# Performance work log

Hardware: AMD Instinct MI355X
Metric: run time of the kernel (lower is better)

The kernel has to match this reference:

```python
import jax, jax.numpy as jnp
import numpy as np

N_NODES = 100000


def _gcn_layer(x, W, b, src, dst, inv_sqrt_deg):
    # transform first (cheaper when out_dim <= in_dim), then normalized aggregate
    h = x @ W  # [N, out]
    coeff = (inv_sqrt_deg[src] * inv_sqrt_deg[dst])[:, None]  # [E,1] sym norm
    msgs = h[src] * coeff  # [E, out]
    agg = jax.ops.segment_sum(msgs, dst, num_segments=N_NODES)  # [N, out]
    return agg + b


def setup_inputs() -> dict:
    key = jax.random.key(0)
    ks = jax.random.split(key, 8)
    n, e = N_NODES, 1600000
    x = jax.random.normal(ks[0], (n, 256), dtype=jnp.float32)
    src = jax.random.randint(ks[1], (e,), 0, n)
    dst = jax.random.randint(ks[2], (e,), 0, n)
    W1 = jax.random.normal(ks[3], (256, 128), dtype=jnp.float32) * 0.05
    b1 = jax.random.normal(ks[4], (128,), dtype=jnp.float32) * 0.05
    W2 = jax.random.normal(ks[5], (128, 40), dtype=jnp.float32) * 0.05
    b2 = jax.random.normal(ks[6], (40,), dtype=jnp.float32) * 0.05
    return {"x": x, "src": src, "dst": dst, "W1": W1, "b1": b1, "W2": W2, "b2": b2}


def reference(x, src, dst, W1, b1, W2, b2):
    # degree-based symmetric normalization D^{-1/2} A D^{-1/2}
    ones = jnp.ones(src.shape, dtype=x.dtype)
    deg = jax.ops.segment_sum(ones, dst, num_segments=N_NODES)
    inv_sqrt_deg = jnp.where(deg > 0, jax.lax.rsqrt(jnp.maximum(deg, 1.0)), 0.0)
    h = _gcn_layer(x, W1, b1, src, dst, inv_sqrt_deg)
    h = jax.nn.relu(h)
    h = _gcn_layer(h, W2, b2, src, dst, inv_sqrt_deg)
    return h
```

## Files before the change

### kernel.cpp

```cpp
#include <hip/hip_runtime.h>
#include <hip/hip_bf16.h>


#define CHUNK   4096
#define NPB     512
#define NBUCK   196
#define BBCAP   9216

typedef __bf16 bf16x8 __attribute__((ext_vector_type(8)));
typedef float floatx4 __attribute__((ext_vector_type(4)));

__device__ inline unsigned short f2bf(float f) {
    unsigned u = __float_as_uint(f);
    u += 0x7FFF + ((u >> 16) & 1);
    return (unsigned short)(u >> 16);
}
__device__ inline float bflo(unsigned p) { return __uint_as_float(p << 16); }
__device__ inline float bfhi(unsigned p) { return __uint_as_float(p & 0xFFFF0000u); }

__global__ __launch_bounds__(256) void k_part(const int* __restrict__ src,
                                              const int* __restrict__ dst,
                                              int* __restrict__ gcursor,
                                              unsigned* __restrict__ buckets, int E) {
    __shared__ unsigned srec[CHUNK];
    __shared__ unsigned char sb8[CHUNK];
    __shared__ int hist[NBUCK];
    __shared__ int lbase[NBUCK];
    __shared__ int gbase[NBUCK];
    __shared__ int scanbuf[256];
    int t = threadIdx.x;
    int base = blockIdx.x * CHUNK;
    int cnt = min(CHUNK, E - base);
    for (int i = t; i < NBUCK; i += 256) hist[i] = 0;
    __syncthreads();

    unsigned rec[16];
    unsigned br[16];
    bool valid[4];
    #pragma unroll
    for (int k = 0; k < 4; ++k) {
        int e0 = k * 1024 + t * 4;
        valid[k] = (e0 < cnt);
        if (valid[k]) {
            int4 s4 = *(const int4*)&src[base + e0];
            int4 d4 = *(const int4*)&dst[base + e0];
            int ss[4] = {s4.x, s4.y, s4.z, s4.w};
            int dd[4] = {d4.x, d4.y, d4.z, d4.w};
            #pragma unroll
            for (int j = 0; j < 4; ++j) {
                int b = dd[j] >> 9;
                int r = atomicAdd(&hist[b], 1);
                rec[k * 4 + j] = (unsigned)ss[j] | ((unsigned)(dd[j] & 511) << 17);
                br[k * 4 + j] = (unsigned)b | ((unsigned)r << 8);
            }
        }
    }
    __syncthreads();
    scanbuf[t] = (t < NBUCK) ? hist[t] : 0;
    __syncthreads();
    for (int s = 1; s < 256; s <<= 1) {
        int v = (t >= s) ? scanbuf[t - s] : 0;
        __syncthreads();
        scanbuf[t] += v;
        __syncthreads();
    }
    if (t < NBUCK) {
        lbase[t] = scanbuf[t] - hist[t];
        gbase[t] = atomicAdd(&gcursor[t], hist[t]);
    }
    __syncthreads();
    #pragma unroll
    for (int k = 0; k < 4; ++k) {
        if (valid[k]) {
            #pragma unroll
            for (int j = 0; j < 4; ++j) {
                unsigned b = br[k * 4 + j] & 255u;
                unsigned r = br[k * 4 + j] >> 8;
                int p = lbase[b] + (int)r;
                srec[p] = rec[k * 4 + j];
                sb8[p] = (unsigned char)b;
            }
        }
    }
    __syncthreads();
    for (int i = t; i < cnt; i += 256) {
        int b = sb8[i];
        int pos = gbase[b] + (i - lbase[b]);
        if (pos < BBCAP) buckets[(size_t)b * BBCAP + pos] = srec[i];
    }
}

__global__ __launch_bounds__(256) void k_count(const unsigned* __restrict__ buckets,
                                               const int* __restrict__ gcursor,
                                               int* __restrict__ deg, int N) {
    __shared__ int hist[NPB];
    int b = blockIdx.x;
    for (int i = threadIdx.x; i < NPB; i += 256) hist[i] = 0;
    __syncthreads();
    int cnt = min(gcursor[b], BBCAP);
    const unsigned* bk = &buckets[(size_t)b * BBCAP];
    for (int i = threadIdx.x; i < cnt; i += 256)
        atomicAdd(&hist[bk[i] >> 17], 1);
    __syncthreads();
    int node0 = b << 9;
    for (int i = threadIdx.x; i < NPB; i += 256)
        if (node0 + i < N) deg[node0 + i] = hist[i];
}

__global__ void k_isd_offsets(const int* __restrict__ deg, float* __restrict__ isd,
                              int* __restrict__ offsets, int* __restrict__ counter, int N) {
    int n = blockIdx.x * blockDim.x + threadIdx.x;
    int lane = threadIdx.x & 63;
    int d = (n < N) ? deg[n] : 0;
    if (n <= N) isd[n] = (d > 0) ? rsqrtf((float)d) : 0.f;
    int dp = (d + 15) & ~15;
    int pref = dp;
    #pragma unroll
    for (int sh = 1; sh < 64; sh <<= 1) {
        int t = __shfl_up(pref, sh);
        if (lane >= sh) pref += t;
    }
    int total = __shfl(pref, 63);
    int base = 0;
    if (lane == 63) base = atomicAdd(counter, total);
    base = __shfl(base, 63);
    if (n < N) offsets[n] = base + pref - dp;
}

__global__ __launch_bounds__(256) void k_place(const unsigned* __restrict__ buckets,
                                               const int* __restrict__ gcursor,
                                               const int* __restrict__ offsets,
                                               const int* __restrict__ deg,
                                               int* __restrict__ csr, int N) {
    __shared__ int cur[NPB];
    int b = blockIdx.x;
    int node0 = b << 9;
    for (int i = threadIdx.x; i < NPB; i += 256)
        cur[i] = (node0 + i < N) ? offsets[node0 + i] : 0;
    __syncthreads();
    int cnt = min(gcursor[b], BBCAP);
    const unsigned* bk = &buckets[(size_t)b * BBCAP];
    for (int i = threadIdx.x; i < cnt; i += 256) {
        unsigned r = bk[i];
        int p = atomicAdd(&cur[r >> 17], 1);
        csr[p] = (int)(r & 0x1FFFFu);
    }
    __syncthreads();
    for (int i = threadIdx.x; i < NPB; i += 256) {
        int n = node0 + i;
        if (n < N) {
            int d = deg[n];
            int st = offsets[n] + d;
            int en = offsets[n] + ((d + 15) & ~15);
            for (int p = st; p < en; ++p) csr[p] = N;
        }
    }
}

__global__ void k_prep_w1(const float* __restrict__ W1, unsigned short* __restrict__ w1s,
                          unsigned* __restrict__ h2z) {
    if (blockIdx.x == 0 && threadIdx.x < 36) h2z[threadIdx.x] = 0;
    int flat = blockIdx.x * 256 + threadIdx.x;
    int kt = flat >> 9;
    int nt = (flat >> 6) & 7;
    int lane = flat & 63;
    int kbase = kt * 32 + ((lane >> 4) << 3);
    int n = nt * 16 + (lane & 15);
    unsigned short v[8];
    #pragma unroll
    for (int j = 0; j < 8; ++j) v[j] = f2bf(W1[(size_t)(kbase + j) * 128 + n]);
    unsigned short* d = &w1s[(size_t)flat * 8];
    *(short4*)(d)     = make_short4(v[0], v[1], v[2], v[3]);
    *(short4*)(d + 4) = make_short4(v[4], v[5], v[6], v[7]);
}

__global__ __launch_bounds__(256) void k_gemm1(const float* __restrict__ X,
                                               const unsigned short* __restrict__ w1s,
                                               const float* __restrict__ isd,
                                               unsigned short* __restrict__ H, int N) {
    __shared__ __align__(16) unsigned short smem[8192];
    unsigned short* sA = smem;
    unsigned short* sB = smem + 2048;
    int tid = threadIdx.x;
    int lane = tid & 63;
    int wave = tid >> 6;
    int wr = wave >> 1;
    int wc = wave & 1;
    int m0 = blockIdx.x * 64;

    floatx4 acc[2][4] = {};

    for (int kt = 0; kt < 8; ++kt) {
        #pragma unroll
        for (int i = 0; i < 2; ++i) {
            int f = tid * 2 + i;
            int row = f >> 3;
            int c4 = (f & 7) * 4;
            float4 v = make_float4(0.f, 0.f, 0.f, 0.f);
            int grow = m0 + row;
            if (grow < N) v = *(const float4*)&X[(size_t)grow * 256 + kt * 32 + c4];
            int mt = row >> 4;
            int flane = (row & 15) | ((c4 >> 3) << 4);
            int j0 = c4 & 7;
            unsigned short* d = &sA[(size_t)(mt * 64 + flane) * 8 + j0];
            *(short4*)d = make_short4(f2bf(v.x), f2bf(v.y), f2bf(v.z), f2bf(v.w));
        }
        {
            const float4* srcp = (const float4*)&w1s[(size_t)kt * 4096];
            float4* dstp = (float4*)sB;
            dstp[tid] = srcp[tid];
            dstp[tid + 256] = srcp[tid + 256];
        }
        __syncthreads();
        bf16x8 a[2], b[4];
        #pragma unroll
        for (int p = 0; p < 2; ++p)
            a[p] = *(const bf16x8*)&sA[(size_t)((wr * 2 + p) * 64 + lane) * 8];
        #pragma unroll
        for (int q = 0; q < 4; ++q)
            b[q] = *(const bf16x8*)&sB[(size_t)((wc * 4 + q) * 64 + lane) * 8];
        #pragma unroll
        for (int p = 0; p < 2; ++p)
            #pragma unroll
            for (int q = 0; q < 4; ++q)
                acc[p][q] = __builtin_amdgcn_mfma_f32_16x16x32_bf16(a[p], b[q], acc[p][q], 0, 0, 0);
        __syncthreads();
    }
    float sc[2][4];
    #pragma unroll
    for (int p = 0; p < 2; ++p)
        #pragma unroll
        for (int r = 0; r < 4; ++r) {
            int g = m0 + wr * 32 + p * 16 + ((lane >> 4) << 2) + r;
            sc[p][r] = isd[g > N ? N : g];
        }
    #pragma unroll
    for (int p = 0; p < 2; ++p)
        #pragma unroll
        for (int q = 0; q < 4; ++q)
            #pragma unroll
            for (int r = 0; r < 4; ++r) {
                int rl = wr * 32 + p * 16 + ((lane >> 4) << 2) + r;
                int c = wc * 64 + q * 16 + (lane & 15);
                smem[rl * 128 + c] = f2bf(acc[p][q][r] * sc[p][r]);
            }
    __syncthreads();
    #pragma unroll
    for (int i = 0; i < 4; ++i) {
        int f = tid + i * 256;
        int row = f >> 4;
        int c8 = (f & 15) * 8;
        int grow = m0 + row;
        if (grow <= N)
            *(float4*)&H[(size_t)grow * 128 + c8] = *(const float4*)&smem[row * 128 + c8];
    }
}

__global__ __launch_bounds__(256) void k_agg1(const unsigned* __restrict__ Hu,
                                              const int* __restrict__ csr,
                                              const float* __restrict__ isd,
                                              const int* __restrict__ offsets,
                                              const int* __restrict__ deg,
                                              const float* __restrict__ b1,
                                              unsigned* __restrict__ H1u, int N) {
    int node = __builtin_amdgcn_readfirstlane((blockIdx.x * blockDim.x + threadIdx.x) >> 6);
    int lane = threadIdx.x & 63;
    if (node >= N) return;
    int start = offsets[node];
    int nb = (deg[node] + 15) >> 4;
    float isdn = isd[node];
    float acc0 = 0.f, acc1 = 0.f;
    for (int ib = 0; ib < nb; ++ib) {
        int b0 = start + ib * 16;
        int s[16];
        #pragma unroll
        for (int j = 0; j < 16; ++j) s[j] = csr[b0 + j];
        unsigned p[16];
        #pragma unroll
        for (int j = 0; j < 16; ++j) p[j] = Hu[(size_t)s[j] * 64 + lane];
        #pragma unroll
        for (int j = 0; j < 16; ++j) {
            acc0 += bflo(p[j]);
            acc1 += bfhi(p[j]);
        }
    }
    float r0 = fmaxf(fmaf(isdn, acc0, b1[2 * lane]), 0.f);
    float r1 = fmaxf(fmaf(isdn, acc1, b1[2 * lane + 1]), 0.f);
    H1u[(size_t)node * 64 + lane] = (unsigned)f2bf(r0) | ((unsigned)f2bf(r1) << 16);
}

__global__ __launch_bounds__(256) void k_gemm2(const unsigned short* __restrict__ H1,
                                               const float* __restrict__ W2,
                                               const float* __restrict__ isd,
                                               unsigned short* __restrict__ H2, int N) {
    __shared__ float sH[64][132];
    __shared__ float sW[128 * 40];
    int tid = threadIdx.x;
    int block_row = blockIdx.x * 64;
    for (int i = tid; i < 64 * 16; i += 256) {
        int r = i >> 4;
        int c8 = (i & 15) * 8;
        int grow = block_row + r;
        uint4 v = make_uint4(0, 0, 0, 0);
        if (grow < N) v = *(const uint4*)&H1[(size_t)grow * 128 + c8];
        float* d = &sH[r][c8];
        d[0] = bflo(v.x); d[1] = bfhi(v.x);
        d[2] = bflo(v.y); d[3] = bfhi(v.y);
        d[4] = bflo(v.z); d[5] = bfhi(v.z);
        d[6] = bflo(v.w); d[7] = bfhi(v.w);
    }
    for (int i = tid; i < 1280; i += 256)
        *(float4*)&sW[i * 4] = *(const float4*)&W2[(size_t)i * 4];
    __syncthreads();

    int row = tid >> 2;
    int c0 = (tid & 3) * 10;
    float acc[10] = {};
    for (int k = 0; k < 128; ++k) {
        float hv = sH[row][k];
        #pragma unroll
        for (int j = 0; j < 5; ++j) {
            float2 wv = *(const float2*)&sW[k * 40 + c0 + 2 * j];
            acc[2 * j]     = fmaf(hv, wv.x, acc[2 * j]);
            acc[2 * j + 1] = fmaf(hv, wv.y, acc[2 * j + 1]);
        }
    }
    int grow = block_row + row;
    if (grow < N) {
        float scn = isd[grow];
        unsigned* o = (unsigned*)&H2[(size_t)grow * 40 + c0];
        #pragma unroll
        for (int j = 0; j < 5; ++j)
            o[j] = (unsigned)f2bf(acc[2 * j] * scn) |
                   ((unsigned)f2bf(acc[2 * j + 1] * scn) << 16);
    }
}

__global__ __launch_bounds__(256) void k_agg2(const unsigned* __restrict__ Hu2,
                                              const int* __restrict__ csr,
                                              const float* __restrict__ isd,
                                              const int* __restrict__ offsets,
                                              const int* __restrict__ deg,
                                              const float* __restrict__ b2,
                                              float* __restrict__ out, int N) {
    int node = __builtin_amdgcn_readfirstlane((blockIdx.x * blockDim.x + threadIdx.x) >> 6);
    int lane = threadIdx.x & 63;
    if (node >= N) return;
    int start = offsets[node];
    int nb = (deg[node] + 15) >> 4;
    float isdn = isd[node];
    int sub = lane >> 5;
    int c = lane & 31;
    float acc0 = 0.f, acc1 = 0.f;
    for (int ib = 0; ib < nb; ++ib) {
        int b0 = start + ib * 16;
        #pragma unroll
        for (int j = 0; j < 8; ++j) {
            int s = csr[b0 + (j << 1) + sub];
            unsigned q = Hu2[(size_t)s * 20 + c];
            acc0 += bflo(q);
            acc1 += bfhi(q);
        }
    }
    acc0 += __shfl(acc0, lane + 32);
    acc1 += __shfl(acc1, lane + 32);
    if (lane < 20)
        *(float2*)&out[(size_t)node * 40 + 2 * lane] =
            make_float2(fmaf(isdn, acc0, b2[2 * lane]), fmaf(isdn, acc1, b2[2 * lane + 1]));
}

extern "C" void kernel_launch(void* const* d_in, const int* in_sizes, int n_in,
                              void* d_out, int out_size, void* d_ws, size_t ws_size,
                              hipStream_t stream) {
    const float* x  = (const float*)d_in[0];
    const int*  src = (const int*)d_in[1];
    const int*  dst = (const int*)d_in[2];
    const float* W1 = (const float*)d_in[3];
    const float* b1 = (const float*)d_in[4];
    const float* W2 = (const float*)d_in[5];
    const float* b2 = (const float*)d_in[6];
    float* out = (float*)d_out;

    const int N = in_sizes[0] / 256;
    const int E = in_sizes[1];

    char* w = (char*)d_ws;
    auto alloc = [&](size_t bytes) -> void* {
        void* p = (void*)w;
        w += (bytes + 15) & ~(size_t)15;
        return p;
    };
    int*      gcursor = (int*)alloc(256 * 4);
    int*      counter = (int*)alloc(16);
    int*      deg     = (int*)alloc((size_t)N * 4);
    float*    isd     = (float*)alloc((size_t)(N + 1) * 4);
    int*      offsets = (int*)alloc((size_t)(N + 1) * 4);
    unsigned* buckets = (unsigned*)alloc((size_t)NBUCK * BBCAP * 4);
    int*      csr     = (int*)alloc((size_t)(E + 16 * (size_t)N) * 4);
    unsigned short* w1s = (unsigned short*)alloc(32768 * 2);
    unsigned short* h   = (unsigned short*)alloc((size_t)(N + 1) * 128 * 2);
    unsigned short* h1  = (unsigned short*)alloc((size_t)N * 128 * 2);
    unsigned short* h2  = (unsigned short*)alloc(((size_t)(N + 1) * 20 + 16) * 4);

    hipMemsetAsync(gcursor, 0, 256 * 4 + 16, stream);

    int nchunk = (E + CHUNK - 1) / CHUNK;
    k_part<<<nchunk, 256, 0, stream>>>(src, dst, gcursor, buckets, E);
    k_count<<<NBUCK, 256, 0, stream>>>(buckets, gcursor, deg, N);
    k_isd_offsets<<<(N + 256) / 256, 256, 0, stream>>>(deg, isd, offsets, counter, N);
    k_place<<<NBUCK, 256, 0, stream>>>(buckets, gcursor, offsets, deg, csr, N);
    k_prep_w1<<<16, 256, 0, stream>>>(W1, w1s, (unsigned*)h2 + (size_t)N * 20);
    k_gemm1<<<(N + 63) / 64, 256, 0, stream>>>(x, w1s, isd, h, N);
    k_agg1<<<(N + 3) / 4, 256, 0, stream>>>((const unsigned*)h, csr, isd, offsets, deg,
                                            b1, (unsigned*)h1, N);
    k_gemm2<<<(N + 63) / 64, 256, 0, stream>>>(h1, W2, isd, h2, N);
    k_agg2<<<(N + 3) / 4, 256, 0, stream>>>((const unsigned*)h2, csr, isd, offsets, deg,
                                            b2, out, N);
}
```

Measured before the change: 408.4 us.

## Fuse graph preprocessing kernels and run CSR placement concurrently with GEMM1

Degree counting moves into the partition kernel as global atomics, and the W1 prep blocks become extra blocks of that kernel. Offset scan, isd and CSR placement merge into one kernel whose remaining blocks run GEMM1, which now computes its row scales from deg itself. This cuts the launch count from six to two and lets the irregular CSR build overlap the dense GEMM. The cost is 1.6M scattered global atomics on deg, a larger memset, and offsets that depend on the order buckets grab the shared counter.

Result: slower. 432.8 us (+6.0%).

```diff
diff --git a/kernel.cpp b/kernel.cpp
--- a/kernel.cpp
+++ b/kernel.cpp
@@ -18,17 +18,39 @@
 __device__ inline float bflo(unsigned p) { return __uint_as_float(p << 16); }
 __device__ inline float bfhi(unsigned p) { return __uint_as_float(p & 0xFFFF0000u); }
 
-__global__ __launch_bounds__(256) void k_part(const int* __restrict__ src,
-                                              const int* __restrict__ dst,
-                                              int* __restrict__ gcursor,
-                                              unsigned* __restrict__ buckets, int E) {
+__global__ __launch_bounds__(256) void k_f1(const int* __restrict__ src,
+                                            const int* __restrict__ dst,
+                                            int* __restrict__ gcursor,
+                                            unsigned* __restrict__ buckets,
+                                            int* __restrict__ deg,
+                                            int E, int nchunk,
+                                            const float* __restrict__ W1,
+                                            unsigned short* __restrict__ w1s,
+                                            unsigned* __restrict__ h2z) {
+    int t = threadIdx.x;
+    if ((int)blockIdx.x >= nchunk) {
+        int pb = blockIdx.x - nchunk;
+        if (pb == 0 && t < 36) h2z[t] = 0;
+        int flat = pb * 256 + t;
+        int kt = flat >> 9;
+        int nt = (flat >> 6) & 7;
+        int lane = flat & 63;
+        int kbase = kt * 32 + ((lane >> 4) << 3);
+        int n = nt * 16 + (lane & 15);
+        unsigned short v[8];
+        #pragma unroll
+        for (int j = 0; j < 8; ++j) v[j] = f2bf(W1[(size_t)(kbase + j) * 128 + n]);
+        unsigned short* d = &w1s[(size_t)flat * 8];
+        *(short4*)(d)     = make_short4(v[0], v[1], v[2], v[3]);
+        *(short4*)(d + 4) = make_short4(v[4], v[5], v[6], v[7]);
+        return;
+    }
     __shared__ unsigned srec[CHUNK];
     __shared__ unsigned char sb8[CHUNK];
     __shared__ int hist[NBUCK];
     __shared__ int lbase[NBUCK];
     __shared__ int gbase[NBUCK];
     __shared__ int scanbuf[256];
-    int t = threadIdx.x;
     int base = blockIdx.x * CHUNK;
     int cnt = min(CHUNK, E - base);
     for (int i = t; i < NBUCK; i += 256) hist[i] = 0;
@@ -50,6 +72,7 @@
             for (int j = 0; j < 4; ++j) {
                 int b = dd[j] >> 9;
                 int r = atomicAdd(&hist[b], 1);
+                atomicAdd(&deg[dd[j]], 1);
                 rec[k * 4 + j] = (unsigned)ss[j] | ((unsigned)(dd[j] & 511) << 17);
                 br[k * 4 + j] = (unsigned)b | ((unsigned)r << 8);
             }
@@ -90,103 +113,78 @@
     }
 }
 
-__global__ __launch_bounds__(256) void k_count(const unsigned* __restrict__ buckets,
-                                               const int* __restrict__ gcursor,
-                                               int* __restrict__ deg, int N) {
-    __shared__ int hist[NPB];
-    int b = blockIdx.x;
-    for (int i = threadIdx.x; i < NPB; i += 256) hist[i] = 0;
-    __syncthreads();
-    int cnt = min(gcursor[b], BBCAP);
-    const unsigned* bk = &buckets[(size_t)b * BBCAP];
-    for (int i = threadIdx.x; i < cnt; i += 256)
-        atomicAdd(&hist[bk[i] >> 17], 1);
-    __syncthreads();
-    int node0 = b << 9;
-    for (int i = threadIdx.x; i < NPB; i += 256)
-        if (node0 + i < N) deg[node0 + i] = hist[i];
-}
-
-__global__ void k_isd_offsets(const int* __restrict__ deg, float* __restrict__ isd,
-                              int* __restrict__ offsets, int* __restrict__ counter, int N) {
-    int n = blockIdx.x * blockDim.x + threadIdx.x;
-    int lane = threadIdx.x & 63;
-    int d = (n < N) ? deg[n] : 0;
-    if (n <= N) isd[n] = (d > 0) ? rsqrtf((float)d) : 0.f;
-    int dp = (d + 15) & ~15;
-    int pref = dp;
-    #pragma unroll
-    for (int sh = 1; sh < 64; sh <<= 1) {
-        int t = __shfl_up(pref, sh);
-        if (lane >= sh) pref += t;
-    }
-    int total = __shfl(pref, 63);
-    int base = 0;
-    if (lane == 63) base = atomicAdd(counter, total);
-    base = __shfl(base, 63);
-    if (n < N) offsets[n] = base + pref - dp;
-}
-
-__global__ __launch_bounds__(256) void k_place(const unsigned* __restrict__ buckets,
-                                               const int* __restrict__ gcursor,
-                                               const int* __restrict__ offsets,
-                                               const int* __restrict__ deg,
-                                               int* __restrict__ csr, int N) {
-    __shared__ int cur[NPB];
-    int b = blockIdx.x;
-    int node0 = b << 9;
-    for (int i = threadIdx.x; i < NPB; i += 256)
-        cur[i] = (node0 + i < N) ? offsets[node0 + i] : 0;
-    __syncthreads();
-    int cnt = min(gcursor[b], BBCAP);
-    const unsigned* bk = &buckets[(size_t)b * BBCAP];
-    for (int i = threadIdx.x; i < cnt; i += 256) {
-        unsigned r = bk[i];
-        int p = atomicAdd(&cur[r >> 17], 1);
-        csr[p] = (int)(r & 0x1FFFFu);
-    }
-    __syncthreads();
-    for (int i = threadIdx.x; i < NPB; i += 256) {
-        int n = node0 + i;
-        if (n < N) {
-            int d = deg[n];
-            int st = offsets[n] + d;
-            int en = offsets[n] + ((d + 15) & ~15);
-            for (int p = st; p < en; ++p) csr[p] = N;
-        }
-    }
-}
-
-__global__ void k_prep_w1(const float* __restrict__ W1, unsigned short* __restrict__ w1s,
-                          unsigned* __restrict__ h2z) {
-    if (blockIdx.x == 0 && threadIdx.x < 36) h2z[threadIdx.x] = 0;
-    int flat = blockIdx.x * 256 + threadIdx.x;
-    int kt = flat >> 9;
-    int nt = (flat >> 6) & 7;
-    int lane = flat & 63;
-    int kbase = kt * 32 + ((lane >> 4) << 3);
-    int n = nt * 16 + (lane & 15);
-    unsigned short v[8];
-    #pragma unroll
-    for (int j = 0; j < 8; ++j) v[j] = f2bf(W1[(size_t)(kbase + j) * 128 + n]);
-    unsigned short* d = &w1s[(size_t)flat * 8];
-    *(short4*)(d)     = make_short4(v[0], v[1], v[2], v[3]);
-    *(short4*)(d + 4) = make_short4(v[4], v[5], v[6], v[7]);
-}
-
-__global__ __launch_bounds__(256) void k_gemm1(const float* __restrict__ X,
-                                               const unsigned short* __restrict__ w1s,
-                                               const float* __restrict__ isd,
-                                               unsigned short* __restrict__ H, int N) {
-    __shared__ __align__(16) unsigned short smem[8192];
+__global__ __launch_bounds__(256) void k_f2(const unsigned* __restrict__ buckets,
+                                            const int* __restrict__ gcursor,
+                                            const int* __restrict__ deg,
+                                            int* __restrict__ counter,
+                                            int* __restrict__ offsets,
+                                            float* __restrict__ isd,
+                                            int* __restrict__ csr,
+                                            const float* __restrict__ X,
+                                            const unsigned short* __restrict__ w1s,
+                                            unsigned short* __restrict__ H, int N) {
+    __shared__ __align__(16) unsigned char SH[16384];
+    int tid = threadIdx.x;
+    if ((int)blockIdx.x < NBUCK) {
+        int* s_off = (int*)SH;
+        int* s_deg = (int*)(SH + 2048);
+        int* cur   = (int*)(SH + 4096);
+        int* sb    = (int*)(SH + 6144);
+        int* sbase = (int*)(SH + 7168);
+        int b = blockIdx.x;
+        int node0 = b << 9;
+        int i0 = tid * 2;
+        int na = node0 + i0, nb = node0 + i0 + 1;
+        int da = (na < N) ? deg[na] : 0;
+        int db = (nb < N) ? deg[nb] : 0;
+        int dpa = (da + 15) & ~15, dpb = (db + 15) & ~15;
+        sb[tid] = dpa + dpb;
+        __syncthreads();
+        for (int s = 1; s < 256; s <<= 1) {
+            int v = (tid >= s) ? sb[tid - s] : 0;
+            __syncthreads();
+            sb[tid] += v;
+            __syncthreads();
+        }
+        int excl = sb[tid] - (dpa + dpb);
+        if (tid == 0) *sbase = atomicAdd(counter, sb[255]);
+        if (b == 0 && tid == 1) isd[N] = 0.f;
+        __syncthreads();
+        int offa = *sbase + excl;
+        int offb = offa + dpa;
+        if (na < N) { offsets[na] = offa; isd[na] = (da > 0) ? rsqrtf((float)da) : 0.f; }
+        if (nb < N) { offsets[nb] = offb; isd[nb] = (db > 0) ? rsqrtf((float)db) : 0.f; }
+        s_off[i0] = offa; s_off[i0 + 1] = offb;
+        s_deg[i0] = da;   s_deg[i0 + 1] = db;
+        cur[i0] = offa;   cur[i0 + 1] = offb;
+        __syncthreads();
+        int cnt = min(gcursor[b], BBCAP);
+        const unsigned* bk = &buckets[(size_t)b * BBCAP];
+        for (int i = tid; i < cnt; i += 256) {
+            unsigned r = bk[i];
+            int p = atomicAdd(&cur[r >> 17], 1);
+            csr[p] = (int)(r & 0x1FFFFu);
+        }
+        __syncthreads();
+        for (int i = tid; i < NPB; i += 256) {
+            int n = node0 + i;
+            if (n < N) {
+                int d = s_deg[i];
+                int st = s_off[i] + d;
+                int en = s_off[i] + ((d + 15) & ~15);
+                for (int p = st; p < en; ++p) csr[p] = N;
+            }
+        }
+        return;
+    }
+    unsigned short* smem = (unsigned short*)SH;
     unsigned short* sA = smem;
     unsigned short* sB = smem + 2048;
-    int tid = threadIdx.x;
     int lane = tid & 63;
     int wave = tid >> 6;
     int wr = wave >> 1;
     int wc = wave & 1;
-    int m0 = blockIdx.x * 64;
+    int m0 = (blockIdx.x - NBUCK) * 64;
 
     floatx4 acc[2][4] = {};
 
@@ -232,7 +230,12 @@
         #pragma unroll
         for (int r = 0; r < 4; ++r) {
             int g = m0 + wr * 32 + p * 16 + ((lane >> 4) << 2) + r;
-            sc[p][r] = isd[g > N ? N : g];
+            float s = 0.f;
+            if (g < N) {
+                int dv = deg[g];
+                s = (dv > 0) ? rsqrtf((float)dv) : 0.f;
+            }
+            sc[p][r] = s;
         }
     #pragma unroll
     for (int p = 0; p < 2; ++p)
@@ -402,18 +405,17 @@
     unsigned short* h1  = (unsigned short*)alloc((size_t)N * 128 * 2);
     unsigned short* h2  = (unsigned short*)alloc(((size_t)(N + 1) * 20 + 16) * 4);
 
-    hipMemsetAsync(gcursor, 0, 256 * 4 + 16, stream);
+    hipMemsetAsync(gcursor, 0, 256 * 4 + 16 + (size_t)N * 4, stream);
 
     int nchunk = (E + CHUNK - 1) / CHUNK;
-    k_part<<<nchunk, 256, 0, stream>>>(src, dst, gcursor, buckets, E);
-    k_count<<<NBUCK, 256, 0, stream>>>(buckets, gcursor, deg, N);
-    k_isd_offsets<<<(N + 256) / 256, 256, 0, stream>>>(deg, isd, offsets, counter, N);
-    k_place<<<NBUCK, 256, 0, stream>>>(buckets, gcursor, offsets, deg, csr, N);
-    k_prep_w1<<<16, 256, 0, stream>>>(W1, w1s, (unsigned*)h2 + (size_t)N * 20);
-    k_gemm1<<<(N + 63) / 64, 256, 0, stream>>>(x, w1s, isd, h, N);
+    int G1 = (N + 63) / 64;
+    k_f1<<<nchunk + 16, 256, 0, stream>>>(src, dst, gcursor, buckets, deg, E, nchunk,
+                                          W1, w1s, (unsigned*)h2 + (size_t)N * 20);
+    k_f2<<<NBUCK + G1, 256, 0, stream>>>(buckets, gcursor, deg, counter, offsets, isd,
+                                         csr, x, w1s, h, N);
     k_agg1<<<(N + 3) / 4, 256, 0, stream>>>((const unsigned*)h, csr, isd, offsets, deg,
                                             b1, (unsigned*)h1, N);
-    k_gemm2<<<(N + 63) / 64, 256, 0, stream>>>(h1, W2, isd, h2, N);
+    k_gemm2<<<G1, 256, 0, stream>>>(h1, W2, isd, h2, N);
     k_agg2<<<(N + 3) / 4, 256, 0, stream>>>((const unsigned*)h2, csr, isd, offsets, deg,
                                             b2, out, N);
 }
```
